# Optimization experiments

Measured on AMD Instinct MI355X. Metric: run time of the kernel, lower is better.

## Reference

```python
import jax, jax.numpy as jnp
import numpy as np

WH, WW = 8, 8          # window height/width
NUM_HEADS = 12


def _rel_tables():
    # continuous relative coords table, shape (1, 2*WH-1, 2*WW-1, 2)
    rh = np.arange(-(WH - 1), WH, dtype=np.float32)
    rw = np.arange(-(WW - 1), WW, dtype=np.float32)
    t = np.expand_dims(np.transpose(np.stack(np.meshgrid(rh, rw)), (1, 2, 0)), axis=0)
    t[:, :, :, 0] /= WH - 1
    t[:, :, :, 1] /= WW - 1
    t *= 8
    table = np.sign(t) * np.log2(np.abs(t) + 1.0) / np.log2(8)
    # relative position index, shape (WH*WW, WH*WW), values in [0, (2WH-1)*(2WW-1))
    ch = np.arange(WH)
    cw = np.arange(WW)
    x, y = np.meshgrid(ch, cw)
    coords = np.stack([y, x]).reshape(2, -1)
    rc = coords[:, :, None] - coords[:, None, :]
    rc = np.transpose(rc, (1, 2, 0))
    rc[:, :, 0] += WH - 1
    rc[:, :, 1] += WW - 1
    rc[:, :, 0] *= 2 * WW - 1
    idx = rc.sum(-1)
    return jnp.asarray(table, dtype=jnp.float32), jnp.asarray(idx, dtype=jnp.int32)


_REL_TABLE, _REL_IDX = _rel_tables()


def setup_inputs() -> dict:
    key = jax.random.key(0)
    ks = jax.random.split(key, 10)
    B_, N, C = 1152, 64, 384
    s = 1.0 / np.sqrt(C)
    return {
        "x": jax.random.normal(ks[0], (B_, N, C), jnp.float32),
        "mask": jnp.zeros((B_, N, N), jnp.float32),  # nW == B_ (B=1)
        "wq": jax.random.normal(ks[1], (C, C), jnp.float32) * s,
        "bq": jnp.zeros((C,), jnp.float32),
        "wk": jax.random.normal(ks[2], (C, C), jnp.float32) * s,
        "wv": jax.random.normal(ks[3], (C, C), jnp.float32) * s,
        "bv": jnp.zeros((C,), jnp.float32),
        "cpb_w1": jax.random.normal(ks[4], (2, 512), jnp.float32) * 0.5,
        "cpb_b1": jnp.zeros((512,), jnp.float32),
        "cpb_w2": jax.random.normal(ks[5], (512, NUM_HEADS), jnp.float32) * (1.0 / np.sqrt(512)),
        "cpb_b2": jnp.zeros((NUM_HEADS,), jnp.float32),
        "tau": jax.random.normal(ks[6], (1, NUM_HEADS, 1, 1), jnp.float32) * 0.02,
        "wproj": jax.random.normal(ks[7], (C, C), jnp.float32) * s,
        "bproj": jnp.zeros((C,), jnp.float32),
    }


def reference(x, mask, wq, bq, wk, wv, bv, cpb_w1, cpb_b1, cpb_w2, cpb_b2, tau, wproj, bproj):
    B_, N, C = x.shape
    H = NUM_HEADS
    Dh = C // H

    def heads(t):  # (B_, N, C) -> (B_, H, N, Dh)
        return jnp.transpose(t.reshape(B_, N, H, Dh), (0, 2, 1, 3))

    q = heads(x @ wq + bq)
    k = heads(x @ wk)
    v = heads(x @ wv + bv)

    # cosine attention: normalize by |q||k|, clamp denominator
    qn = jnp.linalg.norm(q, axis=-1)  # (B_, H, N)
    kn = jnp.linalg.norm(k, axis=-1)
    denom = jnp.maximum(qn[..., :, None] * kn[..., None, :], 1e-6)
    logit_scale = jnp.maximum(tau + jnp.log(10.0), 0.01)  # (1, H, 1, 1)
    attn = jnp.einsum('bhnd,bhmd->bhnm', q, k) / denom * logit_scale

    # continuous position bias via small MLP + gather by relative index
    tb = jax.nn.relu(_REL_TABLE @ cpb_w1 + cpb_b1) @ cpb_w2 + cpb_b2  # (1,15,15,H)
    tb = tb.reshape(-1, H)  # (225, H)
    bias = tb[_REL_IDX.reshape(-1)].reshape(N, N, H)
    bias = 16.0 * jax.nn.sigmoid(jnp.transpose(bias, (2, 0, 1)))  # (H, N, N)
    attn = attn + bias[None]

    nW = mask.shape[0]
    attn = (attn.reshape(B_ // nW, nW, H, N, N) + mask[None, :, None]).reshape(B_, H, N, N)
    attn = jax.nn.softmax(attn, axis=-1)

    out = jnp.transpose(jnp.einsum('bhnm,bhmd->bhnd', attn, v), (0, 2, 1, 3)).reshape(B_, N, C)
    return out @ wproj + bproj
```

## Files before the change

kernel.cpp:

```cpp
#include <hip/hip_runtime.h>
#include <math.h>

#define NB   1152
#define NTOK 64
#define NC   384
#define NH   12
#define NDH  32

typedef short short8 __attribute__((ext_vector_type(8)));
typedef float f32x4  __attribute__((ext_vector_type(4)));

__device__ __forceinline__ unsigned short f2bf(float f) {
    unsigned int u = __builtin_bit_cast(unsigned int, f);
    unsigned int r = u + 0x7fffu + ((u >> 16) & 1u);
    return (unsigned short)(r >> 16);
}
__device__ __forceinline__ unsigned int pack2(float lo, float hi) {
    return (unsigned int)f2bf(lo) | ((unsigned int)f2bf(hi) << 16);
}
__device__ __forceinline__ float bf2f(unsigned short h) {
    return __builtin_bit_cast(float, (unsigned int)h << 16);
}
__device__ __forceinline__ f32x4 mfma_bf16(short8 a, short8 b, f32x4 c) {
    return __builtin_amdgcn_mfma_f32_16x16x32_bf16(a, b, c, 0, 0, 0);
}

__device__ __forceinline__ short8 tile_afrag(const unsigned short* t, int row, int kq) {
    return *(const short8*)((const char*)t + row * 768 + ((kq ^ (row & 7)) << 4));
}

__global__ __launch_bounds__(256) void prep_kernel(
    const float* __restrict__ wq, const float* __restrict__ wk,
    const float* __restrict__ wv, const float* __restrict__ wproj,
    unsigned int* __restrict__ wT, unsigned int* __restrict__ wprojT)
{
    const int o2 = blockIdx.x * 256 + threadIdx.x;
    if (o2 < 221184) {
        const int col = o2 / 192, k2 = o2 % 192, k = k2 * 2;
        const float* src = (col < 384) ? wq : ((col < 768) ? wk : wv);
        const int c = (col < 384) ? col : ((col < 768) ? col - 384 : col - 768);
        const float a = src[(size_t)k * NC + c];
        const float b = src[(size_t)(k + 1) * NC + c];
        wT[col * 192 + k2] = pack2(a, b);
    } else {
        const int o = o2 - 221184;
        const int col = o / 192, k2 = o % 192, k = k2 * 2;
        const float a = wproj[(size_t)k * NC + col];
        const float b = wproj[(size_t)(k + 1) * NC + col];
        wprojT[col * 192 + k2] = pack2(a, b);
    }
}

__global__ __launch_bounds__(64) void cpb_mlp_kernel(
    const float* __restrict__ w1, const float* __restrict__ b1,
    const float* __restrict__ w2, const float* __restrict__ b2,
    float* __restrict__ tbs)
{
    const int p = blockIdx.x;
    const int lane = threadIdx.x;
    const int ip = p / 15, jp = p % 15;
    float u0 = (float)(jp - 7) * (8.0f / 7.0f);
    float u1 = (float)(ip - 7) * (8.0f / 7.0f);
    float s0 = (u0 > 0.f) ? 1.f : ((u0 < 0.f) ? -1.f : 0.f);
    float s1 = (u1 > 0.f) ? 1.f : ((u1 < 0.f) ? -1.f : 0.f);
    float in0 = s0 * log2f(fabsf(u0) + 1.0f) * (1.0f / 3.0f);
    float in1 = s1 * log2f(fabsf(u1) + 1.0f) * (1.0f / 3.0f);

    float a[12];
    #pragma unroll
    for (int m = 0; m < 12; ++m) a[m] = 0.f;
    #pragma unroll
    for (int e = 0; e < 8; ++e) {
        const int j = lane * 8 + e;
        float hh = fmaxf(in0 * w1[j] + in1 * w1[512 + j] + b1[j], 0.0f);
        #pragma unroll
        for (int m = 0; m < 12; ++m) a[m] += hh * w2[j * 12 + m];
    }
    #pragma unroll
    for (int m = 0; m < 12; ++m) {
        #pragma unroll
        for (int off = 1; off < 64; off <<= 1) a[m] += __shfl_xor(a[m], off, 64);
    }
    if (lane < 12) tbs[p * 12 + lane] = a[lane] + b2[lane];
}

__global__ __launch_bounds__(1024) void bias_gather_kernel(
    const float* __restrict__ tbs, float* __restrict__ bias)
{
    const int i = blockIdx.x * 1024 + threadIdx.x;
    if (i >= NH * NTOK * NTOK) return;
    const int h = i >> 12, rem = i & 4095;
    const int ti = rem >> 6, tj = rem & 63;
    const int dr = (ti >> 3) - (tj >> 3);
    const int dc = (ti & 7) - (tj & 7);
    const int p = (dr + 7) * 15 + (dc + 7);
    bias[i] = 16.0f / (1.0f + __expf(-tbs[p * 12 + h]));
}

__global__ __launch_bounds__(256) void attn_kernel(
    const float* __restrict__ x,    const float* __restrict__ mask,
    const float* __restrict__ bq,   const float* __restrict__ bv,
    const float* __restrict__ tau,  const unsigned short* __restrict__ wT,
    const float* __restrict__ bias, float* __restrict__ out)
{
    __shared__ unsigned short xs[64 * 384];
    __shared__ unsigned short qk[5120];
    __shared__ unsigned short vT[32 * 72];
    __shared__ float qn[64], kn[64], rs[64];

    unsigned short* qs = qk;
    unsigned short* ks = qk + 2560;
    unsigned short* Ps = qk;

    const int tid  = threadIdx.x;
    const int b    = blockIdx.x;
    const int w    = tid >> 6;
    const int lane = tid & 63;
    const int quad = lane >> 4;
    const int lq   = lane & 15;
    const int tok0 = w * 16 + quad * 4;
    const int m0   = (w & 1) * 2;
    const int n0   = (w >> 1) * 3;

    unsigned int* xsu = (unsigned int*)xs;

    {
        const int row = tid >> 2;
        const int q4  = tid & 3;
        const float* xr = &x[((size_t)b * NTOK + row) * NC + q4 * 96];
        #pragma unroll
        for (int e = 0; e < 24; ++e) {
            const float4 xv = *(const float4*)&xr[e * 4];
            const int p = q4 * 48 + e * 2;
            const int g = p >> 2;
            const int u = row * 192 + (((g ^ (row & 7)) << 2) | (p & 3));
            uint2 w2;
            w2.x = pack2(xv.x, xv.y);
            w2.y = pack2(xv.z, xv.w);
            *(uint2*)&xsu[u] = w2;
        }
    }
    __syncthreads();

    for (int h = 0; h < NH; ++h) {
        const float ls = fmaxf(tau[h] + 2.302585093f, 0.01f);

        f32x4 acc[2][3];
        #pragma unroll
        for (int mi = 0; mi < 2; ++mi)
            #pragma unroll
            for (int ni = 0; ni < 3; ++ni) acc[mi][ni] = (f32x4){0.f, 0.f, 0.f, 0.f};

        const unsigned short* bp[3];
        #pragma unroll
        for (int ni = 0; ni < 3; ++ni) {
            const int nf = n0 + ni;
            const int col = (nf >> 1) * 384 + h * 32 + (nf & 1) * 16 + lq;
            bp[ni] = wT + (size_t)col * NC + quad * 8;
        }

        for (int ksI = 0; ksI < 12; ++ksI) {
            short8 a0 = tile_afrag(xs, m0 * 16 + lq,       ksI * 4 + quad);
            short8 a1 = tile_afrag(xs, (m0 + 1) * 16 + lq, ksI * 4 + quad);
            #pragma unroll
            for (int ni = 0; ni < 3; ++ni) {
                const short8 bb = *(const short8*)&bp[ni][ksI * 32];
                acc[0][ni] = mfma_bf16(a0, bb, acc[0][ni]);
                acc[1][ni] = mfma_bf16(a1, bb, acc[1][ni]);
            }
        }

        __syncthreads();

        #pragma unroll
        for (int mi = 0; mi < 2; ++mi) {
            const int t0 = (m0 + mi) * 16 + quad * 4;
            #pragma unroll
            for (int ni = 0; ni < 3; ++ni) {
                const int nf = n0 + ni;
                const int d  = (nf & 1) * 16 + lq;
                if (nf < 2) {
                    const float bb = bq[h * 32 + d];
                    #pragma unroll
                    for (int r = 0; r < 4; ++r)
                        qs[(t0 + r) * 40 + d] = f2bf(acc[mi][ni][r] + bb);
                } else if (nf < 4) {
                    #pragma unroll
                    for (int r = 0; r < 4; ++r)
                        ks[(t0 + r) * 40 + d] = f2bf(acc[mi][ni][r]);
                } else {
                    const float bb = bv[h * 32 + d];
                    uint2 u2;
                    u2.x = pack2(acc[mi][ni][0] + bb, acc[mi][ni][1] + bb);
                    u2.y = pack2(acc[mi][ni][2] + bb, acc[mi][ni][3] + bb);
                    *(uint2*)&vT[d * 72 + t0] = u2;
                }
            }
        }
        __syncthreads();

        if (tid < 64) {
            const unsigned int* qu = (const unsigned int*)qs + tid * 20;
            float s = 0.f;
            #pragma unroll
            for (int j = 0; j < 16; ++j) {
                const unsigned int u = qu[j];
                const float a = bf2f((unsigned short)(u & 0xffff));
                const float c = bf2f((unsigned short)(u >> 16));
                s += a * a + c * c;
            }
            qn[tid] = sqrtf(s);
        } else if (tid < 128) {
            const int tt = tid - 64;
            const unsigned int* ku = (const unsigned int*)ks + tt * 20;
            float s = 0.f;
            #pragma unroll
            for (int j = 0; j < 16; ++j) {
                const unsigned int u = ku[j];
                const float a = bf2f((unsigned short)(u & 0xffff));
                const float c = bf2f((unsigned short)(u >> 16));
                s += a * a + c * c;
            }
            kn[tt] = sqrtf(s);
        }
        __syncthreads();

        const short8 aq = *(const short8*)&qs[(w * 16 + lq) * 40 + quad * 8];
        float svf[4][4];
        {
            float qnr[4];
            #pragma unroll
            for (int r = 0; r < 4; ++r) qnr[r] = qn[tok0 + r];
            #pragma unroll
            for (int n = 0; n < 4; ++n) {
                const short8 bk = *(const short8*)&ks[(n * 16 + lq) * 40 + quad * 8];
                const f32x4 sv = mfma_bf16(aq, bk, (f32x4){0.f, 0.f, 0.f, 0.f});
                const int col = n * 16 + lq;
                const float knc = kn[col];
                #pragma unroll
                for (int r = 0; r < 4; ++r) {
                    const int row = tok0 + r;
                    const float den = fmaxf(qnr[r] * knc, 1e-6f);
                    svf[n][r] = sv[r] / den * ls
                              + bias[h * 4096 + row * 64 + col]
                              + mask[(size_t)b * 4096 + row * 64 + col];
                }
            }
        }

        float mx[4], sm[4];
        #pragma unroll
        for (int r = 0; r < 4; ++r) {
            float m = fmaxf(fmaxf(svf[0][r], svf[1][r]), fmaxf(svf[2][r], svf[3][r]));
            #pragma unroll
            for (int off = 1; off < 16; off <<= 1) m = fmaxf(m, __shfl_xor(m, off, 64));
            mx[r] = m; sm[r] = 0.f;
        }
        #pragma unroll
        for (int n = 0; n < 4; ++n)
            #pragma unroll
            for (int r = 0; r < 4; ++r) {
                const float e = __expf(svf[n][r] - mx[r]);
                svf[n][r] = e; sm[r] += e;
            }
        #pragma unroll
        for (int r = 0; r < 4; ++r) {
            #pragma unroll
            for (int off = 1; off < 16; off <<= 1) sm[r] += __shfl_xor(sm[r], off, 64);
        }

        __syncthreads();

        #pragma unroll
        for (int n = 0; n < 4; ++n)
            #pragma unroll
            for (int r = 0; r < 4; ++r)
                Ps[(tok0 + r) * 72 + n * 16 + lq] = f2bf(svf[n][r]);
        if (lq == 0) {
            #pragma unroll
            for (int r = 0; r < 4; ++r) rs[tok0 + r] = sm[r];
        }
        __syncthreads();

        f32x4 oa[2];
        oa[0] = (f32x4){0.f, 0.f, 0.f, 0.f};
        oa[1] = (f32x4){0.f, 0.f, 0.f, 0.f};
        #pragma unroll
        for (int st = 0; st < 2; ++st) {
            const short8 ap = *(const short8*)&Ps[(w * 16 + lq) * 72 + st * 32 + quad * 8];
            #pragma unroll
            for (int n = 0; n < 2; ++n) {
                const short8 bv_ = *(const short8*)&vT[(n * 16 + lq) * 72 + st * 32 + quad * 8];
                oa[n] = mfma_bf16(ap, bv_, oa[n]);
            }
        }
        float rsi[4];
        #pragma unroll
        for (int r = 0; r < 4; ++r) rsi[r] = 1.0f / rs[tok0 + r];
        #pragma unroll
        for (int n = 0; n < 2; ++n)
            #pragma unroll
            for (int r = 0; r < 4; ++r)
                out[((size_t)b * NTOK + tok0 + r) * NC + h * 32 + n * 16 + lq] = oa[n][r] * rsi[r];
    }
}

__global__ __launch_bounds__(256) void proj_kernel(
    const unsigned short* __restrict__ wprojT, const float* __restrict__ bproj,
    float* __restrict__ out)
{
    __shared__ unsigned short as_[64 * 384];
    unsigned int* asu = (unsigned int*)as_;

    const int tid  = threadIdx.x;
    const size_t r0 = (size_t)blockIdx.x * 64;
    const int w    = tid >> 6;
    const int lane = tid & 63;
    const int quad = lane >> 4;
    const int lq   = lane & 15;

    {
        const int row = tid >> 2;
        const int q4  = tid & 3;
        const float* xr = &out[(r0 + row) * NC + q4 * 96];
        #pragma unroll
        for (int e = 0; e < 24; ++e) {
            const float4 xv = *(const float4*)&xr[e * 4];
            const int p = q4 * 48 + e * 2;
            const int g = p >> 2;
            const int u = row * 192 + (((g ^ (row & 7)) << 2) | (p & 3));
            uint2 w2;
            w2.x = pack2(xv.x, xv.y);
            w2.y = pack2(xv.z, xv.w);
            *(uint2*)&asu[u] = w2;
        }
    }
    __syncthreads();

    f32x4 acc[4][6];
    #pragma unroll
    for (int mt = 0; mt < 4; ++mt)
        #pragma unroll
        for (int n = 0; n < 6; ++n) acc[mt][n] = (f32x4){0.f, 0.f, 0.f, 0.f};

    const unsigned short* bp[6];
    #pragma unroll
    for (int n = 0; n < 6; ++n)
        bp[n] = wprojT + (size_t)(w * 96 + n * 16 + lq) * NC + quad * 8;

    for (int ksI = 0; ksI < 12; ++ksI) {
        short8 am[4];
        #pragma unroll
        for (int mt = 0; mt < 4; ++mt)
            am[mt] = tile_afrag(as_, mt * 16 + lq, ksI * 4 + quad);
        #pragma unroll
        for (int n = 0; n < 6; ++n) {
            const short8 bb = *(const short8*)&bp[n][ksI * 32];
            #pragma unroll
            for (int mt = 0; mt < 4; ++mt) acc[mt][n] = mfma_bf16(am[mt], bb, acc[mt][n]);
        }
    }

    float bpv[6];
    #pragma unroll
    for (int n = 0; n < 6; ++n) bpv[n] = bproj[w * 96 + n * 16 + lq];
    #pragma unroll
    for (int mt = 0; mt < 4; ++mt)
        #pragma unroll
        for (int n = 0; n < 6; ++n)
            #pragma unroll
            for (int r = 0; r < 4; ++r)
                out[(r0 + mt * 16 + quad * 4 + r) * NC + w * 96 + n * 16 + lq]
                    = acc[mt][n][r] + bpv[n];
}

extern "C" void kernel_launch(void* const* d_in, const int* in_sizes, int n_in,
                              void* d_out, int out_size, void* d_ws, size_t ws_size,
                              hipStream_t stream) {
    (void)in_sizes; (void)n_in; (void)out_size; (void)ws_size;
    const float* x     = (const float*)d_in[0];
    const float* mask  = (const float*)d_in[1];
    const float* wq    = (const float*)d_in[2];
    const float* bq    = (const float*)d_in[3];
    const float* wk    = (const float*)d_in[4];
    const float* wv    = (const float*)d_in[5];
    const float* bv    = (const float*)d_in[6];
    const float* w1    = (const float*)d_in[7];
    const float* b1    = (const float*)d_in[8];
    const float* w2    = (const float*)d_in[9];
    const float* b2    = (const float*)d_in[10];
    const float* tau   = (const float*)d_in[11];
    const float* wproj = (const float*)d_in[12];
    const float* bproj = (const float*)d_in[13];
    float* out = (float*)d_out;

    unsigned short* wT     = (unsigned short*)d_ws;
    unsigned short* wprojT = (unsigned short*)((char*)d_ws + 884736);
    float*          bias   = (float*)((char*)d_ws + 884736 + 294912);
    float*          tbs    = (float*)((char*)d_ws + 884736 + 294912 + 196608);

    prep_kernel<<<1152, 256, 0, stream>>>(wq, wk, wv, wproj,
                                          (unsigned int*)wT, (unsigned int*)wprojT);
    cpb_mlp_kernel<<<225, 64, 0, stream>>>(w1, b1, w2, b2, tbs);
    bias_gather_kernel<<<48, 1024, 0, stream>>>(tbs, bias);
    attn_kernel<<<NB, 256, 0, stream>>>(x, mask, bq, bv, tau, wT, bias, out);
    proj_kernel<<<NB, 256, 0, stream>>>(wprojT, bproj, out);
}
```

Baseline: 678.6 us.

## Process two heads concurrently per block with 512 threads and register norms

The attention kernel now launches 512 threads and splits them into two groups of four waves, each group handling its own head with double-buffered shared q/k/v tiles. Each wave computes a full 16-row QKV strip for its head, and the q/k norms are computed from fp32 accumulators through shuffle reductions instead of a separate LDS pass. The row-sum is kept in registers, and bias and mask loads are issued before the barrier so they can overlap the GEMM. The aim is to cut barriers per head and raise wave-level parallelism, at the cost of more registers per thread and more shared memory. Norms now come from unrounded fp32 values rather than bf16-rounded ones, which slightly changes numerics.

```diff
diff --git a/kernel.cpp b/kernel.cpp
--- a/kernel.cpp
+++ b/kernel.cpp
@@ -97,20 +97,17 @@
     bias[i] = 16.0f / (1.0f + __expf(-tbs[p * 12 + h]));
 }
 
-__global__ __launch_bounds__(256) void attn_kernel(
+__global__ __launch_bounds__(512, 4) void attn_kernel(
     const float* __restrict__ x,    const float* __restrict__ mask,
     const float* __restrict__ bq,   const float* __restrict__ bv,
     const float* __restrict__ tau,  const unsigned short* __restrict__ wT,
     const float* __restrict__ bias, float* __restrict__ out)
 {
     __shared__ unsigned short xs[64 * 384];
-    __shared__ unsigned short qk[5120];
-    __shared__ unsigned short vT[32 * 72];
-    __shared__ float qn[64], kn[64], rs[64];
-
-    unsigned short* qs = qk;
-    unsigned short* ks = qk + 2560;
-    unsigned short* Ps = qk;
+    __shared__ unsigned short qk2[2][5120];
+    __shared__ unsigned short vT2[2][32 * 72];
+    __shared__ float qn2[2][64];
+    __shared__ float kn2[2][64];
 
     const int tid  = threadIdx.x;
     const int b    = blockIdx.x;
@@ -118,20 +115,20 @@
     const int lane = tid & 63;
     const int quad = lane >> 4;
     const int lq   = lane & 15;
-    const int tok0 = w * 16 + quad * 4;
-    const int m0   = (w & 1) * 2;
-    const int n0   = (w >> 1) * 3;
+    const int mt   = w & 3;
+    const int hw   = w >> 2;
+    const int t0   = mt * 16 + quad * 4;
 
     unsigned int* xsu = (unsigned int*)xs;
 
     {
-        const int row = tid >> 2;
-        const int q4  = tid & 3;
-        const float* xr = &x[((size_t)b * NTOK + row) * NC + q4 * 96];
-        #pragma unroll
-        for (int e = 0; e < 24; ++e) {
-            const float4 xv = *(const float4*)&xr[e * 4];
-            const int p = q4 * 48 + e * 2;
+        const int row = tid >> 3;
+        const int t8  = tid & 7;
+        const float* xr = &x[((size_t)b * NTOK + row) * NC];
+        #pragma unroll
+        for (int e = 0; e < 12; ++e) {
+            const float4 xv = *(const float4*)&xr[(t8 + e * 8) * 4];
+            const int p = (t8 + e * 8) * 2;
             const int g = p >> 2;
             const int u = row * 192 + (((g ^ (row & 7)) << 2) | (p & 3));
             uint2 w2;
@@ -142,109 +139,99 @@
     }
     __syncthreads();
 
-    for (int h = 0; h < NH; ++h) {
-        const float ls = fmaxf(tau[h] + 2.302585093f, 0.01f);
-
-        f32x4 acc[2][3];
-        #pragma unroll
-        for (int mi = 0; mi < 2; ++mi)
-            #pragma unroll
-            for (int ni = 0; ni < 3; ++ni) acc[mi][ni] = (f32x4){0.f, 0.f, 0.f, 0.f};
-
-        const unsigned short* bp[3];
-        #pragma unroll
-        for (int ni = 0; ni < 3; ++ni) {
-            const int nf = n0 + ni;
-            const int col = (nf >> 1) * 384 + h * 32 + (nf & 1) * 16 + lq;
-            bp[ni] = wT + (size_t)col * NC + quad * 8;
+    unsigned short* qs_h = qk2[hw];
+    unsigned short* ks_h = qk2[hw] + 2560;
+    unsigned short* Ps_h = qk2[hw];
+    unsigned short* vT_h = vT2[hw];
+
+    for (int it = 0; it < 6; ++it) {
+        const int h = it * 2 + hw;
+
+        f32x4 acc[6];
+        #pragma unroll
+        for (int j = 0; j < 6; ++j) acc[j] = (f32x4){0.f, 0.f, 0.f, 0.f};
+
+        const unsigned short* bp[6];
+        #pragma unroll
+        for (int j = 0; j < 6; ++j) {
+            const int col = (j >> 1) * 384 + h * 32 + (j & 1) * 16 + lq;
+            bp[j] = wT + (size_t)col * NC + quad * 8;
         }
 
         for (int ksI = 0; ksI < 12; ++ksI) {
-            short8 a0 = tile_afrag(xs, m0 * 16 + lq,       ksI * 4 + quad);
-            short8 a1 = tile_afrag(xs, (m0 + 1) * 16 + lq, ksI * 4 + quad);
-            #pragma unroll
-            for (int ni = 0; ni < 3; ++ni) {
-                const short8 bb = *(const short8*)&bp[ni][ksI * 32];
-                acc[0][ni] = mfma_bf16(a0, bb, acc[0][ni]);
-                acc[1][ni] = mfma_bf16(a1, bb, acc[1][ni]);
-            }
-        }
+            const short8 a = tile_afrag(xs, mt * 16 + lq, ksI * 4 + quad);
+            #pragma unroll
+            for (int j = 0; j < 6; ++j)
+                acc[j] = mfma_bf16(a, *(const short8*)&bp[j][ksI * 32], acc[j]);
+        }
+
+        float biasv[4][4], maskv[4][4];
+        #pragma unroll
+        for (int nt = 0; nt < 4; ++nt)
+            #pragma unroll
+            for (int r = 0; r < 4; ++r) {
+                const int row = t0 + r, col = nt * 16 + lq;
+                biasv[nt][r] = bias[h * 4096 + row * 64 + col];
+                maskv[nt][r] = mask[(size_t)b * 4096 + row * 64 + col];
+            }
 
         __syncthreads();
 
-        #pragma unroll
-        for (int mi = 0; mi < 2; ++mi) {
-            const int t0 = (m0 + mi) * 16 + quad * 4;
-            #pragma unroll
-            for (int ni = 0; ni < 3; ++ni) {
-                const int nf = n0 + ni;
-                const int d  = (nf & 1) * 16 + lq;
-                if (nf < 2) {
-                    const float bb = bq[h * 32 + d];
-                    #pragma unroll
-                    for (int r = 0; r < 4; ++r)
-                        qs[(t0 + r) * 40 + d] = f2bf(acc[mi][ni][r] + bb);
-                } else if (nf < 4) {
-                    #pragma unroll
-                    for (int r = 0; r < 4; ++r)
-                        ks[(t0 + r) * 40 + d] = f2bf(acc[mi][ni][r]);
-                } else {
-                    const float bb = bv[h * 32 + d];
-                    uint2 u2;
-                    u2.x = pack2(acc[mi][ni][0] + bb, acc[mi][ni][1] + bb);
-                    u2.y = pack2(acc[mi][ni][2] + bb, acc[mi][ni][3] + bb);
-                    *(uint2*)&vT[d * 72 + t0] = u2;
+        float qnl[4];
+        {
+            const float bq0 = bq[h * 32 + lq], bq1 = bq[h * 32 + 16 + lq];
+            const float bv0 = bv[h * 32 + lq], bv1 = bv[h * 32 + 16 + lq];
+
+            float qred[4], kred[4];
+            #pragma unroll
+            for (int r = 0; r < 4; ++r) {
+                const float q0 = acc[0][r] + bq0, q1 = acc[1][r] + bq1;
+                qs_h[(t0 + r) * 40 + lq]      = f2bf(q0);
+                qs_h[(t0 + r) * 40 + 16 + lq] = f2bf(q1);
+                ks_h[(t0 + r) * 40 + lq]      = f2bf(acc[2][r]);
+                ks_h[(t0 + r) * 40 + 16 + lq] = f2bf(acc[3][r]);
+                qred[r] = q0 * q0 + q1 * q1;
+                kred[r] = acc[2][r] * acc[2][r] + acc[3][r] * acc[3][r];
+            }
+            uint2 u2;
+            u2.x = pack2(acc[4][0] + bv0, acc[4][1] + bv0);
+            u2.y = pack2(acc[4][2] + bv0, acc[4][3] + bv0);
+            *(uint2*)&vT_h[lq * 72 + t0] = u2;
+            u2.x = pack2(acc[5][0] + bv1, acc[5][1] + bv1);
+            u2.y = pack2(acc[5][2] + bv1, acc[5][3] + bv1);
+            *(uint2*)&vT_h[(16 + lq) * 72 + t0] = u2;
+
+            #pragma unroll
+            for (int r = 0; r < 4; ++r) {
+                #pragma unroll
+                for (int off = 1; off < 16; off <<= 1) {
+                    qred[r] += __shfl_xor(qred[r], off, 64);
+                    kred[r] += __shfl_xor(kred[r], off, 64);
                 }
-            }
-        }
-        __syncthreads();
-
-        if (tid < 64) {
-            const unsigned int* qu = (const unsigned int*)qs + tid * 20;
-            float s = 0.f;
-            #pragma unroll
-            for (int j = 0; j < 16; ++j) {
-                const unsigned int u = qu[j];
-                const float a = bf2f((unsigned short)(u & 0xffff));
-                const float c = bf2f((unsigned short)(u >> 16));
-                s += a * a + c * c;
-            }
-            qn[tid] = sqrtf(s);
-        } else if (tid < 128) {
-            const int tt = tid - 64;
-            const unsigned int* ku = (const unsigned int*)ks + tt * 20;
-            float s = 0.f;
-            #pragma unroll
-            for (int j = 0; j < 16; ++j) {
-                const unsigned int u = ku[j];
-                const float a = bf2f((unsigned short)(u & 0xffff));
-                const float c = bf2f((unsigned short)(u >> 16));
-                s += a * a + c * c;
-            }
-            kn[tt] = sqrtf(s);
-        }
-        __syncthreads();
-
-        const short8 aq = *(const short8*)&qs[(w * 16 + lq) * 40 + quad * 8];
-        float svf[4][4];
-        {
-            float qnr[4];
-            #pragma unroll
-            for (int r = 0; r < 4; ++r) qnr[r] = qn[tok0 + r];
-            #pragma unroll
-            for (int n = 0; n < 4; ++n) {
-                const short8 bk = *(const short8*)&ks[(n * 16 + lq) * 40 + quad * 8];
-                const f32x4 sv = mfma_bf16(aq, bk, (f32x4){0.f, 0.f, 0.f, 0.f});
-                const int col = n * 16 + lq;
-                const float knc = kn[col];
+                qnl[r] = sqrtf(qred[r]);
+            }
+            if (lq == 0) {
                 #pragma unroll
                 for (int r = 0; r < 4; ++r) {
-                    const int row = tok0 + r;
-                    const float den = fmaxf(qnr[r] * knc, 1e-6f);
-                    svf[n][r] = sv[r] / den * ls
-                              + bias[h * 4096 + row * 64 + col]
-                              + mask[(size_t)b * 4096 + row * 64 + col];
+                    qn2[hw][t0 + r] = qnl[r];
+                    kn2[hw][t0 + r] = sqrtf(kred[r]);
                 }
+            }
+        }
+        __syncthreads();
+
+        const float ls = fmaxf(tau[h] + 2.302585093f, 0.01f);
+        const short8 aq = *(const short8*)&qs_h[(mt * 16 + lq) * 40 + quad * 8];
+        float svf[4][4];
+        #pragma unroll
+        for (int nt = 0; nt < 4; ++nt) {
+            const short8 bk = *(const short8*)&ks_h[(nt * 16 + lq) * 40 + quad * 8];
+            const f32x4 sv = mfma_bf16(aq, bk, (f32x4){0.f, 0.f, 0.f, 0.f});
+            const float knc = kn2[hw][nt * 16 + lq];
+            #pragma unroll
+            for (int r = 0; r < 4; ++r) {
+                const float den = fmaxf(qnl[r] * knc, 1e-6f);
+                svf[nt][r] = sv[r] / den * ls + biasv[nt][r] + maskv[nt][r];
             }
         }
 
@@ -257,11 +244,11 @@
             mx[r] = m; sm[r] = 0.f;
         }
         #pragma unroll
-        for (int n = 0; n < 4; ++n)
-            #pragma unroll
-            for (int r = 0; r < 4; ++r) {
-                const float e = __expf(svf[n][r] - mx[r]);
-                svf[n][r] = e; sm[r] += e;
+        for (int nt = 0; nt < 4; ++nt)
+            #pragma unroll
+            for (int r = 0; r < 4; ++r) {
+                const float e = __expf(svf[nt][r] - mx[r]);
+                svf[nt][r] = e; sm[r] += e;
             }
         #pragma unroll
         for (int r = 0; r < 4; ++r) {
@@ -272,14 +259,10 @@
         __syncthreads();
 
         #pragma unroll
-        for (int n = 0; n < 4; ++n)
+        for (int nt = 0; nt < 4; ++nt)
             #pragma unroll
             for (int r = 0; r < 4; ++r)
-                Ps[(tok0 + r) * 72 + n * 16 + lq] = f2bf(svf[n][r]);
-        if (lq == 0) {
-            #pragma unroll
-            for (int r = 0; r < 4; ++r) rs[tok0 + r] = sm[r];
-        }
+                Ps_h[(t0 + r) * 72 + nt * 16 + lq] = f2bf(svf[nt][r]);
         __syncthreads();
 
         f32x4 oa[2];
@@ -287,21 +270,21 @@
         oa[1] = (f32x4){0.f, 0.f, 0.f, 0.f};
         #pragma unroll
         for (int st = 0; st < 2; ++st) {
-            const short8 ap = *(const short8*)&Ps[(w * 16 + lq) * 72 + st * 32 + quad * 8];
+            const short8 ap = *(const short8*)&Ps_h[(mt * 16 + lq) * 72 + st * 32 + quad * 8];
             #pragma unroll
             for (int n = 0; n < 2; ++n) {
-                const short8 bv_ = *(const short8*)&vT[(n * 16 + lq) * 72 + st * 32 + quad * 8];
+                const short8 bv_ = *(const short8*)&vT_h[(n * 16 + lq) * 72 + st * 32 + quad * 8];
                 oa[n] = mfma_bf16(ap, bv_, oa[n]);
             }
         }
         float rsi[4];
         #pragma unroll
-        for (int r = 0; r < 4; ++r) rsi[r] = 1.0f / rs[tok0 + r];
+        for (int r = 0; r < 4; ++r) rsi[r] = 1.0f / sm[r];
         #pragma unroll
         for (int n = 0; n < 2; ++n)
             #pragma unroll
             for (int r = 0; r < 4; ++r)
-                out[((size_t)b * NTOK + tok0 + r) * NC + h * 32 + n * 16 + lq] = oa[n][r] * rsi[r];
+                out[((size_t)b * NTOK + t0 + r) * NC + h * 32 + n * 16 + lq] = oa[n][r] * rsi[r];
     }
 }
 
@@ -403,6 +386,6 @@
                                           (unsigned int*)wT, (unsigned int*)wprojT);
     cpb_mlp_kernel<<<225, 64, 0, stream>>>(w1, b1, w2, b2, tbs);
     bias_gather_kernel<<<48, 1024, 0, stream>>>(tbs, bias);
-    attn_kernel<<<NB, 256, 0, stream>>>(x, mask, bq, bv, tau, wT, bias, out);
+    attn_kernel<<<NB, 512, 0, stream>>>(x, mask, bq, bv, tau, wT, bias, out);
     proj_kernel<<<NB, 256, 0, stream>>>(wprojT, bproj, out);
 }
```

Measured after the change: 868.0 us. 27.9% more time.
